# Kernel optimization log

Measured on AMD Instinct MI355X. Metric: run time of the kernel, lower is better.

Reference implementation:

```python
import jax, jax.numpy as jnp
import numpy as np
from jax import lax

TAGSET_SIZE = 64
START_TAG = TAGSET_SIZE - 2
STOP_TAG = TAGSET_SIZE - 1
NEG_INF = -10000.0


def setup_inputs() -> dict:
    key = jax.random.key(0)
    k_feat, k_trans, k_tags = jax.random.split(key, 3)
    B, S, T = 512, 1024, TAGSET_SIZE
    feats = jax.random.normal(k_feat, (B, S, T), dtype=jnp.float32)
    transitions = jax.random.normal(k_trans, (T, T), dtype=jnp.float32)
    # CRF constraints: nothing transitions FROM anything into START row semantics
    # of the torch code: transitions[START, :] = -1e4 ; transitions[:, STOP] = -1e4
    transitions = transitions.at[START_TAG, :].set(NEG_INF)
    transitions = transitions.at[:, STOP_TAG].set(NEG_INF)
    tags = jax.random.randint(k_tags, (B, S), 0, T - 2, dtype=jnp.int64)
    mask = jnp.ones((B, S), dtype=jnp.int32)
    return {"feats": feats, "transitions": transitions, "tags": tags, "mask": mask}


def _forward_alg(feats, transitions, maskf):
    # feats: (B,S,T), maskf: (B,S) float
    B, S, T = feats.shape
    init = jnp.full((B, T), NEG_INF, dtype=feats.dtype).at[:, START_TAG].set(0.0)

    def step(fv, xs):
        feat, m = xs  # feat: (B,T), m: (B,)
        # next_tag_var[b, next, prev] = fv[b,prev] + trans[next,prev] + feat[b,next]
        nxt = jax.nn.logsumexp(
            fv[:, None, :] + transitions[None, :, :] + feat[:, :, None], axis=2
        )
        m1 = m[:, None]
        return nxt * m1 + fv * (1.0 - m1), None

    fv, _ = lax.scan(step, init, (feats.transpose(1, 0, 2), maskf.T))
    terminal = fv + transitions[STOP_TAG][None, :]
    return jax.nn.logsumexp(terminal, axis=1)  # (B,)


def _score_sentence(feats, transitions, tags, maskf):
    B, S, T = feats.shape
    tags_ext = jnp.concatenate(
        [jnp.full((B, 1), START_TAG, dtype=tags.dtype), tags], axis=1
    )  # (B, S+1)
    cur = tags_ext[:, 1:]   # (B,S)
    prev = tags_ext[:, :-1]  # (B,S)
    emit = jnp.take_along_axis(feats, cur[:, :, None], axis=2)[:, :, 0]  # (B,S)
    trans = transitions[cur, prev]  # (B,S)
    score = jnp.sum((emit + trans) * maskf, axis=1)
    last_idx = maskf.sum(axis=1).astype(jnp.int32)  # index into tags_ext
    last_tags = jnp.take_along_axis(tags_ext, last_idx[:, None].astype(tags.dtype), axis=1)[:, 0]
    return score + transitions[STOP_TAG, last_tags]


def reference(feats, transitions, tags, mask):
    maskf = mask.astype(feats.dtype)
    forward_score = _forward_alg(feats, transitions, maskf)
    gold_score = _score_sentence(feats, transitions, tags, maskf)
    return jnp.mean(forward_score - gold_score)
```

## Files before the change

kernel.cpp:

```cpp
#include <hip/hip_runtime.h>

#define START_TAG 62
#define STOP_TAG 63
#define BATCH 512
#define SLEN 1024
#define NCHAIN 64
#define RD 16
#define AH 8
#define SLOTB 4096

typedef float vf4 __attribute__((ext_vector_type(4)));
typedef short short8 __attribute__((ext_vector_type(8)));

__device__ __forceinline__ unsigned pk_bf16(float lo, float hi) {
  return __builtin_amdgcn_perm(__float_as_uint(hi), __float_as_uint(lo), 0x07060302u);
}
__device__ __forceinline__ short bf16_rne(float x) {
  unsigned u = __float_as_uint(x);
  u += 0x7FFFu + ((u >> 16) & 1u);
  return (short)(u >> 16);
}
__device__ __forceinline__ vf4 mfma16(short8 a, short8 b, vf4 c) {
  return __builtin_amdgcn_mfma_f32_16x16x32_bf16(a, b, c, 0, 0, 0);
}
__device__ __forceinline__ void async16(const void* g, void* l) {
  __builtin_amdgcn_global_load_lds((const __attribute__((address_space(1))) unsigned*)g,
                                   (__attribute__((address_space(3))) unsigned*)l, 16, 0, 0);
}

template<int DIR>
__device__ __forceinline__ void load_A(const float* __restrict__ trans, short8 A[4][2],
                                       int q, int col) {
  const int mrow = 16 * (col >> 2) + (col & 3);
  #pragma unroll
  for (int t = 0; t < 4; ++t) {
    #pragma unroll
    for (int c = 0; c < 2; ++c) {
      short8 a;
      #pragma unroll
      for (int j = 0; j < 8; ++j) {
        int R = mrow + 4 * t, K = 16 * q + 8 * c + j;
        float tv = (DIR == 0) ? trans[R * 64 + K] : trans[K * 64 + R];
        a[j] = bf16_rne(__expf(tv));
      }
      A[t][c] = a;
    }
  }
}

template<int DIR>
__device__ __forceinline__ void epilogue(float* __restrict__ ws, const float W[16],
                                         float C, int g, int lane, int q, int col) {
  float* slab = ws + (size_t)(g * 2 + DIR) * 1024;
  #pragma unroll
  for (int t4 = 0; t4 < 4; ++t4) {
    vf4 o = {W[t4 * 4], W[t4 * 4 + 1], W[t4 * 4 + 2], W[t4 * 4 + 3]};
    *(vf4*)(slab + lane * 16 + t4 * 4) = o;
  }
  if (q == 0) ws[65536 + (g * 2 + DIR) * 16 + col] = C;
}

template<int DIR>
__device__ __forceinline__ void chain_fast(const float* __restrict__ feats,
                                           const float* __restrict__ trans,
                                           float* __restrict__ ws, char* smem, int g) {
  const int lane = threadIdx.x & 63;
  const int q = lane >> 4, col = lane & 15;
  const int b = g * 16 + col;

  short8 A[4][2];
  load_A<DIR>(trans, A, q, col);

  float W[16];
  if (DIR == 0) {
    #pragma unroll
    for (int i = 0; i < 16; ++i) W[i] = 0.f;
    if (q == 3) W[14] = 1.f;
  } else {
    #pragma unroll
    for (int i = 0; i < 16; ++i) W[i] = __expf(trans[STOP_TAG * 64 + 16 * q + i]);
  }

  const char* gb = (const char*)feats + (size_t)b * 262144 + (size_t)q * 64;

  asm volatile("s_waitcnt vmcnt(0)" ::: "memory");
  #pragma unroll
  for (int p = 0; p < AH; ++p) {
    size_t s = (DIR == 0) ? (size_t)p : (size_t)(1023 - p);
    #pragma unroll
    for (int v = 0; v < 4; ++v)
      async16(gb + s * 256 + v * 16, smem + p * SLOTB + v * 1024);
  }
  asm volatile("s_waitcnt vmcnt(28)" ::: "memory");
  vf4 cur[4];
  #pragma unroll
  for (int v = 0; v < 4; ++v)
    cur[v] = *(const vf4*)(smem + v * 1024 + lane * 16);

  float C = 0.f, zpend = 1.f;

  for (int bk = 0; bk < 32; ++bk) {
    #pragma unroll
    for (int u = 0; u < 16; ++u) {
      const int j = bk * 16 + u;
      int jp = j + AH; if (jp > 511) jp = 511;
      const size_t sp = (DIR == 0) ? (size_t)jp : (size_t)(1023 - jp);
      const int wslot = (u + AH) & 15;
      #pragma unroll
      for (int v = 0; v < 4; ++v)
        async16(gb + sp * 256 + v * 16, smem + wslot * SLOTB + v * 1024);
      asm volatile("s_waitcnt vmcnt(28)" ::: "memory");
      const int rslot = (u + 1) & 15;
      vf4 nxt[4];
      #pragma unroll
      for (int v = 0; v < 4; ++v)
        nxt[v] = *(const vf4*)(smem + rslot * SLOTB + v * 1024 + lane * 16);

      float e[16];
      #pragma unroll
      for (int v = 0; v < 4; ++v)
        #pragma unroll
        for (int i = 0; i < 4; ++i) e[v * 4 + i] = __expf(cur[v][i]);

      float P[16];
      #pragma unroll
      for (int i = 0; i < 16; ++i) P[i] = (DIR == 0) ? W[i] : W[i] * e[i];

      union { unsigned uu[4]; short8 s8; } B0, B1;
      B0.uu[0] = pk_bf16(P[0], P[1]);   B0.uu[1] = pk_bf16(P[2], P[3]);
      B0.uu[2] = pk_bf16(P[4], P[5]);   B0.uu[3] = pk_bf16(P[6], P[7]);
      B1.uu[0] = pk_bf16(P[8], P[9]);   B1.uu[1] = pk_bf16(P[10], P[11]);
      B1.uu[2] = pk_bf16(P[12], P[13]); B1.uu[3] = pk_bf16(P[14], P[15]);

      vf4 z4 = {0.f, 0.f, 0.f, 0.f};
      vf4 d0 = mfma16(A[0][0], B0.s8, z4);
      vf4 d1 = mfma16(A[1][0], B0.s8, z4);
      vf4 d2 = mfma16(A[2][0], B0.s8, z4);
      vf4 d3 = mfma16(A[3][0], B0.s8, z4);
      d0 = mfma16(A[0][1], B1.s8, d0);
      d1 = mfma16(A[1][1], B1.s8, d1);
      d2 = mfma16(A[2][1], B1.s8, d2);
      d3 = mfma16(A[3][1], B1.s8, d3);

      #pragma unroll
      for (int i = 0; i < 4; ++i) {
        W[i]      = (DIR == 0) ? d0[i] * e[i]      : d0[i];
        W[4 + i]  = (DIR == 0) ? d1[i] * e[4 + i]  : d1[i];
        W[8 + i]  = (DIR == 0) ? d2[i] * e[8 + i]  : d2[i];
        W[12 + i] = (DIR == 0) ? d3[i] * e[12 + i] : d3[i];
      }
      #pragma unroll
      for (int v = 0; v < 4; ++v) cur[v] = nxt[v];

      if ((u & 3) == 3) {
        float rz = __builtin_amdgcn_rcpf(zpend);
        C += __logf(zpend);
        #pragma unroll
        for (int i = 0; i < 16; ++i) W[i] *= rz;
        zpend = __shfl(W[0], col);
      }
    }
  }
  epilogue<DIR>(ws, W, C, g, lane, q, col);
}

template<int DIR>
__device__ __forceinline__ void chain_masked(const float* __restrict__ feats,
                                             const float* __restrict__ trans,
                                             const int* __restrict__ mask,
                                             float* __restrict__ ws, int g) {
  const int lane = threadIdx.x & 63;
  const int q = lane >> 4, col = lane & 15;
  const int b = g * 16 + col;

  short8 A[4][2];
  load_A<DIR>(trans, A, q, col);

  float W[16];
  float C = 0.f;
  if (DIR == 0) {
    #pragma unroll
    for (int i = 0; i < 16; ++i) W[i] = 0.f;
    if (q == 3) W[14] = 1.f;
  } else {
    #pragma unroll
    for (int i = 0; i < 16; ++i) W[i] = __expf(trans[STOP_TAG * 64 + 16 * q + i]);
  }

  const char* gb = (const char*)feats + (size_t)b * 262144 + (size_t)q * 64;
  vf4 cur[4];
  {
    size_t s0 = (DIR == 0) ? 0 : 1023;
    #pragma unroll
    for (int v = 0; v < 4; ++v)
      cur[v] = *(const vf4*)(gb + s0 * 256 + (size_t)v * 16);
  }

  for (int grp = 0; grp < 128; ++grp) {
    #pragma unroll
    for (int u = 0; u < 4; ++u) {
      const int j = grp * 4 + u;
      float e[16];
      #pragma unroll
      for (int v = 0; v < 4; ++v)
        #pragma unroll
        for (int i = 0; i < 4; ++i) e[v * 4 + i] = __expf(cur[v][i]);

      float P[16];
      #pragma unroll
      for (int i = 0; i < 16; ++i) P[i] = (DIR == 0) ? W[i] : W[i] * e[i];

      union { unsigned uu[4]; short8 s8; } B0, B1;
      B0.uu[0] = pk_bf16(P[0], P[1]);   B0.uu[1] = pk_bf16(P[2], P[3]);
      B0.uu[2] = pk_bf16(P[4], P[5]);   B0.uu[3] = pk_bf16(P[6], P[7]);
      B1.uu[0] = pk_bf16(P[8], P[9]);   B1.uu[1] = pk_bf16(P[10], P[11]);
      B1.uu[2] = pk_bf16(P[12], P[13]); B1.uu[3] = pk_bf16(P[14], P[15]);

      vf4 z4 = {0.f, 0.f, 0.f, 0.f};
      vf4 d0 = mfma16(A[0][0], B0.s8, z4);
      vf4 d1 = mfma16(A[1][0], B0.s8, z4);
      vf4 d2 = mfma16(A[2][0], B0.s8, z4);
      vf4 d3 = mfma16(A[3][0], B0.s8, z4);
      d0 = mfma16(A[0][1], B1.s8, d0);
      d1 = mfma16(A[1][1], B1.s8, d1);
      d2 = mfma16(A[2][1], B1.s8, d2);
      d3 = mfma16(A[3][1], B1.s8, d3);

      int sj = (DIR == 0) ? j : 1023 - j;
      int m = mask[b * 1024 + sj];
      int sn = (DIR == 0) ? (j + 1) : 1023 - (j + 1);
      #pragma unroll
      for (int v = 0; v < 4; ++v)
        cur[v] = *(const vf4*)(gb + (size_t)sn * 256 + (size_t)v * 16);

      #pragma unroll
      for (int i = 0; i < 4; ++i) {
        float n0 = (DIR == 0) ? d0[i] * e[i]      : d0[i];
        float n1 = (DIR == 0) ? d1[i] * e[4 + i]  : d1[i];
        float n2 = (DIR == 0) ? d2[i] * e[8 + i]  : d2[i];
        float n3 = (DIR == 0) ? d3[i] * e[12 + i] : d3[i];
        W[i]      = m ? n0 : W[i];
        W[4 + i]  = m ? n1 : W[4 + i];
        W[8 + i]  = m ? n2 : W[8 + i];
        W[12 + i] = m ? n3 : W[12 + i];
      }
    }
    float z = __shfl(W[0], col);
    float rz = __builtin_amdgcn_rcpf(z);
    C += __logf(z);
    #pragma unroll
    for (int i = 0; i < 16; ++i) W[i] *= rz;
  }
  epilogue<DIR>(ws, W, C, g, lane, q, col);
}

__global__ __launch_bounds__(64, 1)
void crf_main(const float* __restrict__ feats, const float* __restrict__ trans,
              const int* __restrict__ tags, const int* __restrict__ mask,
              float* __restrict__ ws) {
  __shared__ char smem[RD * SLOTB];
  const int blk = blockIdx.x;
  if (blk < NCHAIN) {
    const int g = blk >> 1, dir = blk & 1;
    const int lane = threadIdx.x & 63;
    const int q = lane >> 4, col = lane & 15;
    const int b = g * 16 + col;
    const int sB = dir ? 512 : 0;
    int anyz = 0;
    for (int it = 0; it < 32; ++it) {
      int4 v = *(const int4*)(mask + b * 1024 + sB + (it * 4 + q) * 4);
      anyz |= (v.x == 0) | (v.y == 0) | (v.z == 0) | (v.w == 0);
    }
    bool allones = (__ballot(anyz != 0) == 0ull);
    if (allones) {
      if (dir == 0) chain_fast<0>(feats, trans, ws, smem, g);
      else          chain_fast<1>(feats, trans, ws, smem, g);
    } else {
      if (dir == 0) chain_masked<0>(feats, trans, mask, ws, g);
      else          chain_masked<1>(feats, trans, mask, ws, g);
    }
    (void)tags;
  } else {
    const int b = blk - NCHAIN;
    const int* tb = tags + b * SLEN;
    const int* mb = mask + b * SLEN;
    const float* fbg = feats + (size_t)b * 65536;
    float acc = 0.f, cnt = 0.f;
    const int t = threadIdx.x;
    for (int k = 0; k < 16; ++k) {
      int s = t + k * 64;
      int cur = tb[s];
      int prev = (s == 0) ? START_TAG : tb[s - 1];
      float m = (float)mb[s];
      acc += m * (fbg[s * 64 + cur] + trans[cur * 64 + prev]);
      cnt += m;
    }
    #pragma unroll
    for (int o = 1; o < 64; o <<= 1) {
      acc += __shfl_xor(acc, o);
      cnt += __shfl_xor(cnt, o);
    }
    if (t == 0) {
      int last_idx = (int)(cnt + 0.5f);
      int last_tag = (last_idx == 0) ? START_TAG : tb[last_idx - 1];
      ws[66560 + b] = acc + trans[STOP_TAG * 64 + last_tag];
    }
  }
}

__global__ __launch_bounds__(512)
void crf_reduce(const float* __restrict__ ws, float* __restrict__ out) {
  __shared__ float s[512];
  const int t = threadIdx.x;
  const int g = t >> 4, col = t & 15;
  const float* Wf = ws + (size_t)(2 * g) * 1024;
  const float* Wb = ws + (size_t)(2 * g + 1) * 1024;
  float P = 0.f;
  #pragma unroll
  for (int q = 0; q < 4; ++q)
    #pragma unroll
    for (int i = 0; i < 16; ++i)
      P += Wf[(q * 16 + col) * 16 + i] * Wb[(q * 16 + col) * 16 + i];
  float sc = ws[65536 + (2 * g) * 16 + col] + ws[65536 + (2 * g + 1) * 16 + col] + __logf(P);
  s[t] = sc - ws[66560 + t];
  __syncthreads();
  for (int off = 256; off > 0; off >>= 1) {
    if (t < off) s[t] += s[t + off];
    __syncthreads();
  }
  if (t == 0) out[0] = s[0] * (1.f / 512.f);
}

extern "C" void kernel_launch(void* const* d_in, const int* in_sizes, int n_in,
                              void* d_out, int out_size, void* d_ws, size_t ws_size,
                              hipStream_t stream) {
  const float* feats = (const float*)d_in[0];
  const float* trans = (const float*)d_in[1];
  const int* tags = (const int*)d_in[2];
  const int* mask = (const int*)d_in[3];
  float* ws = (float*)d_ws;
  float* out = (float*)d_out;

  crf_main<<<NCHAIN + BATCH, 64, 0, stream>>>(feats, trans, tags, mask, ws);
  crf_reduce<<<1, 512, 0, stream>>>(ws, out);
}
```

Before: 301.6 us.

## Replace LDS async prefetch ring with register FIFO of direct global loads

```diff
diff --git a/kernel.cpp b/kernel.cpp
--- a/kernel.cpp
+++ b/kernel.cpp
@@ -5,9 +5,6 @@
 #define BATCH 512
 #define SLEN 1024
 #define NCHAIN 64
-#define RD 16
-#define AH 8
-#define SLOTB 4096
 
 typedef float vf4 __attribute__((ext_vector_type(4)));
 typedef short short8 __attribute__((ext_vector_type(8)));
@@ -23,10 +20,20 @@
 __device__ __forceinline__ vf4 mfma16(short8 a, short8 b, vf4 c) {
   return __builtin_amdgcn_mfma_f32_16x16x32_bf16(a, b, c, 0, 0, 0);
 }
-__device__ __forceinline__ void async16(const void* g, void* l) {
-  __builtin_amdgcn_global_load_lds((const __attribute__((address_space(1))) unsigned*)g,
-                                   (__attribute__((address_space(3))) unsigned*)l, 16, 0, 0);
-}
+
+#define FIFO_LOAD(slot, addr)                                              \
+  asm volatile("global_load_dwordx4 %0, %4, off\n\t"                       \
+               "global_load_dwordx4 %1, %4, off offset:16\n\t"             \
+               "global_load_dwordx4 %2, %4, off offset:32\n\t"             \
+               "global_load_dwordx4 %3, %4, off offset:48"                 \
+               : "=v"(F[slot][0]), "=v"(F[slot][1]),                       \
+                 "=v"(F[slot][2]), "=v"(F[slot][3])                        \
+               : "v"(addr) : "memory")
+
+#define FIFO_WAIT12(slot)                                                  \
+  asm volatile("s_waitcnt vmcnt(12)"                                       \
+               : "+v"(F[slot][0]), "+v"(F[slot][1]),                       \
+                 "+v"(F[slot][2]), "+v"(F[slot][3]) :: "memory")
 
 template<int DIR>
 __device__ __forceinline__ void load_A(const float* __restrict__ trans, short8 A[4][2],
@@ -63,7 +70,7 @@
 template<int DIR>
 __device__ __forceinline__ void chain_fast(const float* __restrict__ feats,
                                            const float* __restrict__ trans,
-                                           float* __restrict__ ws, char* smem, int g) {
+                                           float* __restrict__ ws, int g) {
   const int lane = threadIdx.x & 63;
   const int q = lane >> 4, col = lane & 15;
   const int b = g * 16 + col;
@@ -82,45 +89,33 @@
   }
 
   const char* gb = (const char*)feats + (size_t)b * 262144 + (size_t)q * 64;
-
+  const ptrdiff_t delta = (DIR == 0) ? 256 : -256;
+
+  vf4 F[4][4];
   asm volatile("s_waitcnt vmcnt(0)" ::: "memory");
   #pragma unroll
-  for (int p = 0; p < AH; ++p) {
-    size_t s = (DIR == 0) ? (size_t)p : (size_t)(1023 - p);
-    #pragma unroll
-    for (int v = 0; v < 4; ++v)
-      async16(gb + s * 256 + v * 16, smem + p * SLOTB + v * 1024);
-  }
-  asm volatile("s_waitcnt vmcnt(28)" ::: "memory");
-  vf4 cur[4];
-  #pragma unroll
-  for (int v = 0; v < 4; ++v)
-    cur[v] = *(const vf4*)(smem + v * 1024 + lane * 16);
+  for (int p = 0; p < 4; ++p) {
+    const char* a = gb + (size_t)((DIR == 0) ? p : 1023 - p) * 256;
+    FIFO_LOAD(p, a);
+  }
+  const char* ap = gb + (size_t)((DIR == 0) ? 4 : 1019) * 256;
 
   float C = 0.f, zpend = 1.f;
 
   for (int bk = 0; bk < 32; ++bk) {
     #pragma unroll
     for (int u = 0; u < 16; ++u) {
-      const int j = bk * 16 + u;
-      int jp = j + AH; if (jp > 511) jp = 511;
-      const size_t sp = (DIR == 0) ? (size_t)jp : (size_t)(1023 - jp);
-      const int wslot = (u + AH) & 15;
-      #pragma unroll
-      for (int v = 0; v < 4; ++v)
-        async16(gb + sp * 256 + v * 16, smem + wslot * SLOTB + v * 1024);
-      asm volatile("s_waitcnt vmcnt(28)" ::: "memory");
-      const int rslot = (u + 1) & 15;
-      vf4 nxt[4];
-      #pragma unroll
-      for (int v = 0; v < 4; ++v)
-        nxt[v] = *(const vf4*)(smem + rslot * SLOTB + v * 1024 + lane * 16);
+      const int sl = u & 3;
+      FIFO_WAIT12(sl);
 
       float e[16];
       #pragma unroll
       for (int v = 0; v < 4; ++v)
         #pragma unroll
-        for (int i = 0; i < 4; ++i) e[v * 4 + i] = __expf(cur[v][i]);
+        for (int i = 0; i < 4; ++i) e[v * 4 + i] = __expf(F[sl][v][i]);
+
+      FIFO_LOAD(sl, ap);
+      ap += delta;
 
       float P[16];
       #pragma unroll
@@ -149,8 +144,6 @@
         W[8 + i]  = (DIR == 0) ? d2[i] * e[8 + i]  : d2[i];
         W[12 + i] = (DIR == 0) ? d3[i] * e[12 + i] : d3[i];
       }
-      #pragma unroll
-      for (int v = 0; v < 4; ++v) cur[v] = nxt[v];
 
       if ((u & 3) == 3) {
         float rz = __builtin_amdgcn_rcpf(zpend);
@@ -161,6 +154,13 @@
       }
     }
   }
+
+  asm volatile("s_waitcnt vmcnt(0)"
+               : "+v"(F[0][0]), "+v"(F[0][1]), "+v"(F[0][2]), "+v"(F[0][3]),
+                 "+v"(F[1][0]), "+v"(F[1][1]), "+v"(F[1][2]), "+v"(F[1][3]),
+                 "+v"(F[2][0]), "+v"(F[2][1]), "+v"(F[2][2]), "+v"(F[2][3]),
+                 "+v"(F[3][0]), "+v"(F[3][1]), "+v"(F[3][2]), "+v"(F[3][3]) :: "memory");
+
   epilogue<DIR>(ws, W, C, g, lane, q, col);
 }
 
@@ -258,7 +258,6 @@
 void crf_main(const float* __restrict__ feats, const float* __restrict__ trans,
               const int* __restrict__ tags, const int* __restrict__ mask,
               float* __restrict__ ws) {
-  __shared__ char smem[RD * SLOTB];
   const int blk = blockIdx.x;
   if (blk < NCHAIN) {
     const int g = blk >> 1, dir = blk & 1;
@@ -273,8 +272,8 @@
     }
     bool allones = (__ballot(anyz != 0) == 0ull);
     if (allones) {
-      if (dir == 0) chain_fast<0>(feats, trans, ws, smem, g);
-      else          chain_fast<1>(feats, trans, ws, smem, g);
+      if (dir == 0) chain_fast<0>(feats, trans, ws, g);
+      else          chain_fast<1>(feats, trans, ws, g);
     } else {
       if (dir == 0) chain_masked<0>(feats, trans, mask, ws, g);
       else          chain_masked<1>(feats, trans, mask, ws, g);
```

New measurement: 299.4 us. Within noise of the previous version (-0.7%).

## Split CRF chain into producer waves and a consumer wave over an LDS ring

Applied to the files above, without the earlier changes.

```diff
diff --git a/kernel.cpp b/kernel.cpp
--- a/kernel.cpp
+++ b/kernel.cpp
@@ -5,8 +5,7 @@
 #define BATCH 512
 #define SLEN 1024
 #define NCHAIN 64
-#define RD 16
-#define AH 8
+#define RING 16
 #define SLOTB 4096
 
 typedef float vf4 __attribute__((ext_vector_type(4)));
@@ -22,10 +21,6 @@
 }
 __device__ __forceinline__ vf4 mfma16(short8 a, short8 b, vf4 c) {
   return __builtin_amdgcn_mfma_f32_16x16x32_bf16(a, b, c, 0, 0, 0);
-}
-__device__ __forceinline__ void async16(const void* g, void* l) {
-  __builtin_amdgcn_global_load_lds((const __attribute__((address_space(1))) unsigned*)g,
-                                   (__attribute__((address_space(3))) unsigned*)l, 16, 0, 0);
 }
 
 template<int DIR>
@@ -61,12 +56,57 @@
 }
 
 template<int DIR>
-__device__ __forceinline__ void chain_fast(const float* __restrict__ feats,
-                                           const float* __restrict__ trans,
-                                           float* __restrict__ ws, char* smem, int g) {
+__device__ __forceinline__ void producer(const float* __restrict__ feats, char* sm,
+                                         int* flags, volatile int* cprog, int g, int pid) {
   const int lane = threadIdx.x & 63;
   const int q = lane >> 4, col = lane & 15;
   const int b = g * 16 + col;
+  const float* fb = feats + (size_t)b * 65536 + q * 16;
+
+  int j = pid - 1;
+  vf4 L[4];
+  {
+    size_t s = (size_t)(DIR ? 1023 - j : j);
+    #pragma unroll
+    for (int v = 0; v < 4; ++v) L[v] = *(const vf4*)(fb + s * 64 + v * 4);
+  }
+  int cp = -1;
+  while (j <= 515) {
+    int nj = j + 3;
+    vf4 N[4] = {L[0], L[1], L[2], L[3]};
+    if (nj <= 515) {
+      int sc = nj > 511 ? 511 : nj;
+      size_t s = (size_t)(DIR ? 1023 - sc : sc);
+      #pragma unroll
+      for (int v = 0; v < 4; ++v) N[v] = *(const vf4*)(fb + s * 64 + v * 4);
+    }
+    if (j >= RING) {
+      while (cp < j - RING) cp = *cprog;
+    }
+    vf4 ev[4];
+    #pragma unroll
+    for (int v = 0; v < 4; ++v)
+      #pragma unroll
+      for (int i = 0; i < 4; ++i) ev[v][i] = __expf(L[v][i]);
+    char* sb = sm + (j & 15) * SLOTB;
+    #pragma unroll
+    for (int v = 0; v < 4; ++v)
+      *(vf4*)(sb + v * 1024 + lane * 16) = ev[v];
+    asm volatile("s_waitcnt lgkmcnt(0)" ::: "memory");
+    if (lane == 0) *(volatile int*)(flags + (j & 15)) = j + 1;
+    #pragma unroll
+    for (int v = 0; v < 4; ++v) L[v] = N[v];
+    j = nj;
+  }
+}
+
+template<int DIR>
+__device__ __forceinline__ void consumer(const float* __restrict__ trans,
+                                         float* __restrict__ ws, char* sm,
+                                         int* flags, int g) {
+  const int lane = threadIdx.x & 63;
+  const int q = lane >> 4, col = lane & 15;
+  const int b = g * 16 + col;
 
   short8 A[4][2];
   load_A<DIR>(trans, A, q, col);
@@ -81,21 +121,14 @@
     for (int i = 0; i < 16; ++i) W[i] = __expf(trans[STOP_TAG * 64 + 16 * q + i]);
   }
 
-  const char* gb = (const char*)feats + (size_t)b * 262144 + (size_t)q * 64;
-
-  asm volatile("s_waitcnt vmcnt(0)" ::: "memory");
-  #pragma unroll
-  for (int p = 0; p < AH; ++p) {
-    size_t s = (DIR == 0) ? (size_t)p : (size_t)(1023 - p);
-    #pragma unroll
-    for (int v = 0; v < 4; ++v)
-      async16(gb + s * 256 + v * 16, smem + p * SLOTB + v * 1024);
-  }
-  asm volatile("s_waitcnt vmcnt(28)" ::: "memory");
-  vf4 cur[4];
+  volatile int* vfl = (volatile int*)flags;
+  while (vfl[0] != 1) {}
+  asm volatile("" ::: "memory");
+  vf4 ereg[4];
   #pragma unroll
   for (int v = 0; v < 4; ++v)
-    cur[v] = *(const vf4*)(smem + v * 1024 + lane * 16);
+    ereg[v] = *(const vf4*)(sm + v * 1024 + lane * 16);
+  int fl_next = vfl[1];
 
   float C = 0.f, zpend = 1.f;
 
@@ -103,28 +136,23 @@
     #pragma unroll
     for (int u = 0; u < 16; ++u) {
       const int j = bk * 16 + u;
-      int jp = j + AH; if (jp > 511) jp = 511;
-      const size_t sp = (DIR == 0) ? (size_t)jp : (size_t)(1023 - jp);
-      const int wslot = (u + AH) & 15;
+      if (fl_next != j + 2) {
+        while (fl_next != j + 2) fl_next = vfl[(u + 1) & 15];
+      }
+      asm volatile("" ::: "memory");
+      const int rs = (u + 1) & 15;
+      vf4 enxt[4];
       #pragma unroll
       for (int v = 0; v < 4; ++v)
-        async16(gb + sp * 256 + v * 16, smem + wslot * SLOTB + v * 1024);
-      asm volatile("s_waitcnt vmcnt(28)" ::: "memory");
-      const int rslot = (u + 1) & 15;
-      vf4 nxt[4];
-      #pragma unroll
-      for (int v = 0; v < 4; ++v)
-        nxt[v] = *(const vf4*)(smem + rslot * SLOTB + v * 1024 + lane * 16);
-
-      float e[16];
+        enxt[v] = *(const vf4*)(sm + rs * SLOTB + v * 1024 + lane * 16);
+      int fl2 = vfl[(u + 2) & 15];
+
+      float P[16];
       #pragma unroll
       for (int v = 0; v < 4; ++v)
         #pragma unroll
-        for (int i = 0; i < 4; ++i) e[v * 4 + i] = __expf(cur[v][i]);
-
-      float P[16];
-      #pragma unroll
-      for (int i = 0; i < 16; ++i) P[i] = (DIR == 0) ? W[i] : W[i] * e[i];
+        for (int i = 0; i < 4; ++i)
+          P[v * 4 + i] = (DIR == 0) ? W[v * 4 + i] : W[v * 4 + i] * ereg[v][i];
 
       union { unsigned uu[4]; short8 s8; } B0, B1;
       B0.uu[0] = pk_bf16(P[0], P[1]);   B0.uu[1] = pk_bf16(P[2], P[3]);
@@ -144,13 +172,15 @@
 
       #pragma unroll
       for (int i = 0; i < 4; ++i) {
-        W[i]      = (DIR == 0) ? d0[i] * e[i]      : d0[i];
-        W[4 + i]  = (DIR == 0) ? d1[i] * e[4 + i]  : d1[i];
-        W[8 + i]  = (DIR == 0) ? d2[i] * e[8 + i]  : d2[i];
-        W[12 + i] = (DIR == 0) ? d3[i] * e[12 + i] : d3[i];
-      }
-      #pragma unroll
-      for (int v = 0; v < 4; ++v) cur[v] = nxt[v];
+        W[i]      = (DIR == 0) ? d0[i] * ereg[0][i] : d0[i];
+        W[4 + i]  = (DIR == 0) ? d1[i] * ereg[1][i] : d1[i];
+        W[8 + i]  = (DIR == 0) ? d2[i] * ereg[2][i] : d2[i];
+        W[12 + i] = (DIR == 0) ? d3[i] * ereg[3][i] : d3[i];
+      }
+
+      fl_next = fl2;
+      #pragma unroll
+      for (int v = 0; v < 4; ++v) ereg[v] = enxt[v];
 
       if ((u & 3) == 3) {
         float rz = __builtin_amdgcn_rcpf(zpend);
@@ -158,6 +188,7 @@
         #pragma unroll
         for (int i = 0; i < 16; ++i) W[i] *= rz;
         zpend = __shfl(W[0], col);
+        if (lane == 0) *(volatile int*)(flags + 16) = j;
       }
     }
   }
@@ -254,16 +285,21 @@
   epilogue<DIR>(ws, W, C, g, lane, q, col);
 }
 
-__global__ __launch_bounds__(64, 1)
+__global__ __launch_bounds__(256, 1)
 void crf_main(const float* __restrict__ feats, const float* __restrict__ trans,
               const int* __restrict__ tags, const int* __restrict__ mask,
               float* __restrict__ ws) {
-  __shared__ char smem[RD * SLOTB];
+  __shared__ char sm[RING * SLOTB + 128];
   const int blk = blockIdx.x;
   if (blk < NCHAIN) {
+    int* flags = (int*)(sm + RING * SLOTB);
     const int g = blk >> 1, dir = blk & 1;
+    const int wv = threadIdx.x >> 6;
     const int lane = threadIdx.x & 63;
     const int q = lane >> 4, col = lane & 15;
+    if (threadIdx.x < 17) flags[threadIdx.x] = (threadIdx.x == 16) ? -1 : 0;
+    __syncthreads();
+
     const int b = g * 16 + col;
     const int sB = dir ? 512 : 0;
     int anyz = 0;
@@ -272,15 +308,25 @@
       anyz |= (v.x == 0) | (v.y == 0) | (v.z == 0) | (v.w == 0);
     }
     bool allones = (__ballot(anyz != 0) == 0ull);
+
     if (allones) {
-      if (dir == 0) chain_fast<0>(feats, trans, ws, smem, g);
-      else          chain_fast<1>(feats, trans, ws, smem, g);
+      if (wv == 0) {
+        if (dir == 0) consumer<0>(trans, ws, sm, flags, g);
+        else          consumer<1>(trans, ws, sm, flags, g);
+      } else {
+        volatile int* cprog = (volatile int*)(flags + 16);
+        if (dir == 0) producer<0>(feats, sm, flags, cprog, g, wv);
+        else          producer<1>(feats, sm, flags, cprog, g, wv);
+      }
     } else {
-      if (dir == 0) chain_masked<0>(feats, trans, mask, ws, g);
-      else          chain_masked<1>(feats, trans, mask, ws, g);
+      if (wv == 0) {
+        if (dir == 0) chain_masked<0>(feats, trans, mask, ws, g);
+        else          chain_masked<1>(feats, trans, mask, ws, g);
+      }
     }
     (void)tags;
   } else {
+    if (threadIdx.x >= 64) return;
     const int b = blk - NCHAIN;
     const int* tb = tags + b * SLEN;
     const int* mb = mask + b * SLEN;
@@ -341,6 +387,6 @@
   float* ws = (float*)d_ws;
   float* out = (float*)d_out;
 
-  crf_main<<<NCHAIN + BATCH, 64, 0, stream>>>(feats, trans, tags, mask, ws);
+  crf_main<<<NCHAIN + BATCH, 256, 0, stream>>>(feats, trans, tags, mask, ws);
   crf_reduce<<<1, 512, 0, stream>>>(ws, out);
 }
```

Result: slower. 316.1 us (+4.8%).
